# Kernel optimization log

Hardware: AMD Instinct MI355X
Metric: run time of the kernel (lower is better)

## Reference

```python
import jax, jax.numpy as jnp
import numpy as np

D_MODEL = 256
GAMMA = 0.9          # ret_D is built in the torch forward but never applied to the output; kept for fidelity notes
SCALE_BASE = 512     # XPOS default
TEMP = 10000.0
TWO_PI = 2.0 * np.pi


def sine_pos_embed(x):
    """DETR-style 1D sine position embedding with an all-ones mask (as in forward).
    x: [B,T,C] -> pos: [1,T,C] (mask is [1,T] ones, so batch dim broadcasts)."""
    T, C = x.shape[1], x.shape[2]
    x_embed = jnp.arange(1, T + 1, dtype=jnp.float32)          # cumsum of ones
    x_embed = x_embed / (x_embed[-1] + 1e-6) * TWO_PI          # normalize=True
    dim_t = TEMP ** (2.0 * (jnp.arange(C) // 2).astype(jnp.float32) / C)
    pos = x_embed[:, None] / dim_t                             # [T,C]
    pos = jnp.stack([jnp.sin(pos[:, 0::2]), jnp.cos(pos[:, 1::2])], axis=2).reshape(T, C)
    return pos[None].astype(x.dtype)


def _dup_interleave(m):
    # [L, d/2] -> [L, d], columns repeated pairwise: [a,b] -> [a,a,b,b]
    return jnp.repeat(m, 2, axis=-1)


def _rotate_every_two(x):
    x1, x2 = x[..., 0::2], x[..., 1::2]
    return jnp.stack([-x2, x1], axis=-1).reshape(x.shape)


def xpos_apply(x, downscale=False):
    """RetNet XPOS rotary embedding. x: [B,L,d]."""
    L, d = x.shape[1], x.shape[2]
    half = d // 2
    scale_vec = (jnp.arange(0, d, 2, dtype=jnp.float32) + 0.4 * d) / (1.4 * d)   # [d/2]
    power = jnp.arange(L, dtype=jnp.float32) / SCALE_BASE
    scale = scale_vec[None, :] ** power[:, None]                                  # [L, d/2]
    inv_freq = 1.0 / (TEMP ** (jnp.arange(half, dtype=jnp.float32) / half))
    sinusoid = jnp.arange(L, dtype=jnp.float32)[:, None] * inv_freq[None, :]      # [L, d/2]
    sin, cos = jnp.sin(sinusoid), jnp.cos(sinusoid)
    if downscale:
        scale = 1.0 / scale
    sin_s = _dup_interleave(sin * scale)[None].astype(x.dtype)   # [1,L,d]
    cos_s = _dup_interleave(cos * scale)[None].astype(x.dtype)
    return x * cos_s + _rotate_every_two(x) * sin_s


def setup_inputs() -> dict:
    key = jax.random.key(0)
    ks = jax.random.split(key, 8)
    B, TXT, VID, D = 16, 32, 2048, D_MODEL
    S = TXT + VID
    inp = {
        "src": jax.random.normal(ks[0], (B, S, D), dtype=jnp.float32),
        "learn_vid_ret": jax.random.normal(ks[1], (VID * VID, 1), dtype=jnp.float32),
        "W_txt_Q": jax.random.normal(ks[2], (D, D), dtype=jnp.float32) / D,
        "W_txt_K": jax.random.normal(ks[3], (D, D), dtype=jnp.float32) / D,
        "W_txt_V": jax.random.normal(ks[4], (D, D), dtype=jnp.float32) / D,
        "W_vid_Q": jax.random.normal(ks[5], (D, D), dtype=jnp.float32) / D,
        "W_vid_K": jax.random.normal(ks[6], (D, D), dtype=jnp.float32) / D,
        "W_vid_V": jax.random.normal(ks[7], (D, D), dtype=jnp.float32) / D,
        "txt_length": TXT,
    }
    return inp


def reference(src, learn_vid_ret, W_txt_Q, W_txt_K, W_txt_V, W_vid_Q, W_vid_K, W_vid_V, txt_length):
    S = src.shape[1]
    vid_length = S - txt_length

    # learned retention mask over the video block
    learn_ret = jax.nn.sigmoid(learn_vid_ret.reshape(vid_length, vid_length))
    diag = jnp.eye(vid_length, dtype=src.dtype)
    video_ret = (1.0 - diag) * learn_ret
    loss_sparsity = jnp.mean(jnp.abs(video_ret))

    # full [S,S] mask: ones everywhere, sigmoid(learned) on the vid-vid block
    ret_mask = jnp.ones((S, S), dtype=src.dtype).at[txt_length:, txt_length:].set(learn_ret)

    txt_mem = src[:, :txt_length]   # [B,TXT,D]
    vid_mem = src[:, txt_length:]   # [B,VID,D]

    pos = sine_pos_embed(txt_mem)   # [1,TXT,D]
    txt_Q = (pos + txt_mem) @ W_txt_Q
    txt_K = (pos + txt_mem) @ W_txt_K
    vid_Q = xpos_apply(vid_mem @ W_vid_Q)
    vid_K = xpos_apply(vid_mem @ W_vid_K, downscale=True)

    Q = jnp.concatenate([txt_Q, vid_Q], axis=1)                  # [B,S,D]
    K = jnp.concatenate([txt_K, vid_K], axis=1)                  # [B,S,D]
    V = jnp.concatenate([txt_mem @ W_txt_V, vid_mem @ W_vid_V], axis=1)

    # retention: QK^T elementwise-masked (no softmax), then weighted V sum
    scores = jnp.einsum('bsd,btd->bst', Q, K) * ret_mask[None]   # [B,S,S]
    out = scores @ V                                             # [B,S,D]
    return out, loss_sparsity
```

## Files before the change

### kernel.cpp

```cpp
#include <hip/hip_runtime.h>

#define B_   16
#define TXT  32
#define VID  2048
#define D_   256
#define S_   2080
#define SP   2176
#define NKT  34
#define GTOT 17424

typedef unsigned short ushort_t;
typedef __attribute__((ext_vector_type(8))) short short8;
typedef __attribute__((ext_vector_type(4))) short short4v;
typedef __attribute__((ext_vector_type(4))) float f32x4;
typedef __attribute__((ext_vector_type(16))) float f32x16;

__device__ __forceinline__ ushort_t f2bf(float f) {
  unsigned u = __builtin_bit_cast(unsigned, f);
  unsigned r = (u + 0x7FFFu + ((u >> 16) & 1u)) >> 16;
  return (ushort_t)r;
}
__device__ __forceinline__ float bf2f(ushort_t h) {
  unsigned u = ((unsigned)h) << 16;
  return __builtin_bit_cast(float, u);
}

__device__ __forceinline__ void g2l16(void* lds, const void* g) {
  __builtin_amdgcn_global_load_lds(
      (const __attribute__((address_space(1))) char*)g,
      (__attribute__((address_space(3))) char*)lds, 16, 0, 0);
}

__device__ __forceinline__ f32x4 mfma16(short8 a, short8 b, f32x4 c) {
  return __builtin_amdgcn_mfma_f32_16x16x32_bf16(a, b, c, 0, 0, 0);
}
__device__ __forceinline__ f32x16 mfma32(short8 a, short8 b, f32x16 c) {
  return __builtin_amdgcn_mfma_f32_32x32x16_bf16(a, b, c, 0, 0, 0);
}


__global__ void prep_kernel(const float* __restrict__ src, const float* __restrict__ learn,
                            const float* __restrict__ Wtq, const float* __restrict__ Wtk,
                            const float* __restrict__ Wtv,
                            const float* __restrict__ Wvq, const float* __restrict__ Wvk,
                            const float* __restrict__ Wvv,
                            ushort_t* __restrict__ Qs, ushort_t* __restrict__ Ks,
                            ushort_t* __restrict__ VTs, ushort_t* __restrict__ sigp,
                            float* __restrict__ tbl, ushort_t* __restrict__ WT,
                            float* __restrict__ loss) {
  __shared__ float shf[64 * 68];
  const int blk = blockIdx.x;
  const int tid = threadIdx.x;

  if (blk < 64) {
    float (*a_s)[256] = (float(*)[256])shf;
    float (*x_s)[256] = (float(*)[256])(shf + 2048);
    const int tg = blk & 3;
    const int b  = blk >> 2;
    const int c  = tid;
    #pragma unroll
    for (int t = 0; t < 8; ++t) {
      int row = tg * 8 + t;
      float x = src[((size_t)b * S_ + row) * D_ + c];
      float xe = (float)(row + 1) * (6.283185307179586f / (32.0f + 1e-6f));
      int i = c >> 1;
      float dimt = powf(10000.0f, (2.0f * (float)i) / 256.0f);
      float ang = xe / dimt;
      float pv = (c & 1) ? cosf(ang) : sinf(ang);
      x_s[t][c] = x;
      a_s[t][c] = x + pv;
    }
    __syncthreads();
    float q[8] = {0,0,0,0,0,0,0,0}, k[8] = {0,0,0,0,0,0,0,0}, v[8] = {0,0,0,0,0,0,0,0};
    for (int kk = 0; kk < 256; ++kk) {
      float wq = Wtq[(size_t)kk * 256 + c];
      float wk = Wtk[(size_t)kk * 256 + c];
      float wv = Wtv[(size_t)kk * 256 + c];
      #pragma unroll
      for (int t = 0; t < 8; ++t) {
        q[t] = fmaf(a_s[t][kk], wq, q[t]);
        k[t] = fmaf(a_s[t][kk], wk, k[t]);
        v[t] = fmaf(x_s[t][kk], wv, v[t]);
      }
    }
    #pragma unroll
    for (int t = 0; t < 8; ++t) {
      int row = tg * 8 + t;
      size_t base = ((size_t)(b * NKT)) << 14;
      size_t sub = (size_t)(c >> 4) * 1024 + row * 16 + (c & 15);
      Qs[base + sub] = f2bf(q[t]);
      Ks[(base + sub) ^ (size_t)(((row >> 2) & 7) << 3)] = f2bf(k[t]);
      VTs[base + (size_t)(row >> 4) * 4096 + c * 16 + (row & 15)] = f2bf(v[t]);
    }
  } else if (blk < 112) {
    float (*t)[68] = (float(*)[68])shf;
    const int m = blk - 64;
    const int k0 = (m & 3) * 64, n0 = ((m >> 2) & 3) * 64, mt = m >> 4;
    const float* W = (mt == 0) ? Wvq : (mt == 1) ? Wvk : Wvv;
    int r = tid >> 4, cq = (tid & 15) * 4;
    #pragma unroll
    for (int mm = 0; mm < 4; ++mm) {
      int k = mm * 16 + r;
      float4 v = *(const float4*)(W + (size_t)(k0 + k) * 256 + n0 + cq);
      t[k][cq] = v.x; t[k][cq + 1] = v.y; t[k][cq + 2] = v.z; t[k][cq + 3] = v.w;
    }
    __syncthreads();
    #pragma unroll
    for (int mm = 0; mm < 4; ++mm) {
      int n = mm * 16 + r;
      short4v h;
      h[0] = (short)f2bf(t[cq + 0][n]);
      h[1] = (short)f2bf(t[cq + 1][n]);
      h[2] = (short)f2bf(t[cq + 2][n]);
      h[3] = (short)f2bf(t[cq + 3][n]);
      *(short4v*)(WT + ((size_t)mt * D_ + n0 + n) * D_ + k0 + cq) = h;
    }
  } else if (blk < 1136) {
    int idx = (blk - 112) * 256 + tid;
    int n = idx >> 7, i = idx & 127;
    float invf = powf(10000.0f, -(float)i / 128.0f);
    float ang = (float)n * invf;
    float s, co;
    sincosf(ang, &s, &co);
    float sv = ((float)(2 * i) + 102.4f) / 358.4f;
    float sc = powf(sv, (float)n / 512.0f);
    float4 r;
    r.x = co * sc; r.y = s * sc; r.z = co / sc; r.w = s / sc;
    *(float4*)(tbl + (size_t)idx * 4) = r;
  } else if (blk < 1328) {
    int i = (blk - 1136) * 256 + tid;
    short8 z = {0, 0, 0, 0, 0, 0, 0, 0};
    int sec = i >> 14;
    int j = i & 16383;
    int bb = j >> 10;
    int rem = j & 1023;
    size_t base = ((size_t)(bb * NKT + 32)) << 14;
    if (sec == 0) {
      int kstep = rem >> 6, ch = rem & 63;
      *(short8*)(Qs + base + kstep * 1024 + 512 + ch * 8) = z;
    } else if (sec == 1) {
      int kstep = rem >> 6, ch = rem & 63;
      *(short8*)(Ks + base + kstep * 1024 + 512 + ch * 8) = z;
    } else {
      *(short8*)(VTs + base + 8192 + rem * 8) = z;
    }
  } else {
    float* red = shf;
    const int base = ((blk - 1328) * 256 + tid) * 8;
    float4 v0 = *(const float4*)(learn + base);
    float4 v1 = *(const float4*)(learn + base + 4);
    float vals[8] = {v0.x, v0.y, v0.z, v0.w, v1.x, v1.y, v1.z, v1.w};
    float acc = 0.f;
    short8 sh;
    #pragma unroll
    for (int j = 0; j < 8; ++j) {
      int idx = base + j;
      float s = 1.0f / (1.0f + expf(-vals[j]));
      sh[j] = (short)f2bf(s);
      int rr = idx >> 11, cc = idx & 2047;
      if (rr != cc) acc += s;
    }
    *(short8*)(sigp + base) = sh;
    red[tid] = acc;
    __syncthreads();
    #pragma unroll
    for (int st = 128; st > 0; st >>= 1) {
      if (tid < st) red[tid] += red[tid + st];
      __syncthreads();
    }
    if (tid == 0) atomicAdd(loss, red[0] * (1.0f / 4194304.0f));
  }
}

__global__ void cvt_kernel(const float* __restrict__ src, ushort_t* __restrict__ srcb) {
  int i = blockIdx.x * 256 + threadIdx.x;
  int b = i >> 16;
  int rem = i & 65535;
  int row = rem >> 5, c8 = (rem & 31) * 8;
  const float* p = src + ((size_t)b * S_ + TXT + row) * D_ + c8;
  float4 v0 = *(const float4*)p;
  float4 v1 = *(const float4*)(p + 4);
  short8 h;
  h[0] = (short)f2bf(v0.x); h[1] = (short)f2bf(v0.y); h[2] = (short)f2bf(v0.z); h[3] = (short)f2bf(v0.w);
  h[4] = (short)f2bf(v1.x); h[5] = (short)f2bf(v1.y); h[6] = (short)f2bf(v1.z); h[7] = (short)f2bf(v1.w);
  *(short8*)(srcb + ((size_t)b * VID + row) * D_ + c8) = h;
}

template <int MODE>
__global__ __launch_bounds__(256, 2) void vid_gemm(
    const float* __restrict__ src, const ushort_t* __restrict__ srcb,
    const ushort_t* __restrict__ WT, const float* __restrict__ tbl,
    ushort_t* __restrict__ Qs, ushort_t* __restrict__ Ks, ushort_t* __restrict__ VTs) {
  __shared__ __align__(16) ushort_t ldsA[64 * 64];
  __shared__ __align__(16) ushort_t ldsB[64 * 64];

  const int rt = blockIdx.x;
  const int b  = blockIdx.y;
  const int ct = blockIdx.z;
  const int nt = ct >> 2;
  const int n0 = (ct & 3) * 64;
  const int tid = threadIdx.x;
  const int wv = tid >> 6, lane = tid & 63, l15 = lane & 15, l4 = lane >> 4;

  f32x4 acc[4];
  #pragma unroll
  for (int t2 = 0; t2 < 4; ++t2) { acc[t2][0] = 0.f; acc[t2][1] = 0.f; acc[t2][2] = 0.f; acc[t2][3] = 0.f; }

  for (int kk = 0; kk < 256; kk += 64) {
    if (MODE == 1) {
      #pragma unroll
      for (int m = 0; m < 2; ++m) {
        int p = (m * 256 + tid) * 16;
        int r = p >> 7;
        int cb = (p & 127) ^ ((r & 7) << 4);
        g2l16((char*)ldsA + p,
              (const char*)(srcb + ((size_t)b * VID + rt * 64 + r) * D_ + kk) + cb);
      }
    } else {
      #pragma unroll
      for (int m = 0; m < 4; ++m) {
        int q = m * 256 + tid;
        int r = q >> 4;
        int kc = (q & 15) * 4;
        const float4 v = *(const float4*)(src + ((size_t)b * S_ + TXT + rt * 64 + r) * D_ + kk + kc);
        short4v h;
        h[0] = (short)f2bf(v.x); h[1] = (short)f2bf(v.y);
        h[2] = (short)f2bf(v.z); h[3] = (short)f2bf(v.w);
        int off = ((r << 7) + (kc << 1)) ^ ((r & 7) << 4);
        *(short4v*)((char*)ldsA + off) = h;
      }
    }
    #pragma unroll
    for (int m = 0; m < 2; ++m) {
      int p = (m * 256 + tid) * 16;
      int nl = p >> 7;
      int c = (p & 127) ^ ((nl & 7) << 4);
      g2l16((char*)ldsB + p, (const char*)(WT + ((size_t)nt * D_ + n0 + nl) * D_ + kk) + c);
    }
    __syncthreads();
    #pragma unroll
    for (int ks = 0; ks < 2; ++ks) {
      int ar = wv * 16 + l15;
      int aoff = ((ar << 7) + ((ks * 32 + l4 * 8) << 1)) ^ ((ar & 7) << 4);
      short8 av = *(const short8*)((const char*)ldsA + aoff);
      #pragma unroll
      for (int t2 = 0; t2 < 4; ++t2) {
        int nl = t2 * 16 + l15;
        int boff = ((nl << 7) + ((ks * 32 + l4 * 8) << 1)) ^ ((nl & 7) << 4);
        short8 bv = *(const short8*)((const char*)ldsB + boff);
        acc[t2] = mfma16(av, bv, acc[t2]);
      }
    }
    __syncthreads();
  }

  const int rowl = wv * 16 + l4 * 4;
  if (nt < 2) {
    #pragma unroll
    for (int t2 = 0; t2 < 4; ++t2) {
      int c = n0 + t2 * 16 + l15;
      #pragma unroll
      for (int r = 0; r < 4; ++r) {
        int n = rt * 64 + rowl + r;
        float x = acc[t2][r];
        float xp = __shfl_xor(x, 1);
        const float4 tb = *(const float4*)(tbl + ((size_t)n * 128 + (c >> 1)) * 4);
        float cs = (nt == 0) ? tb.x : tb.z;
        float ss = (nt == 0) ? tb.y : tb.w;
        float val = (c & 1) ? fmaf(x, cs, xp * ss) : fmaf(x, cs, -xp * ss);
        int rowg = TXT + n;
        size_t idx = (((size_t)(b * NKT + (rowg >> 6))) << 14)
                   + (size_t)(c >> 4) * 1024 + (rowg & 63) * 16 + (c & 15);
        if (nt == 0) Qs[idx] = f2bf(val);
        else         Ks[idx ^ (size_t)(((rowg >> 2) & 7) << 3)] = f2bf(val);
      }
    }
  } else {
    #pragma unroll
    for (int t2 = 0; t2 < 4; ++t2)
      #pragma unroll
      for (int r = 0; r < 4; ++r) {
        int rr = rowl + r;
        int cc = t2 * 16 + l15;
        int off = ((rr << 7) + (cc << 1)) ^ ((rr & 7) << 4);
        *(ushort_t*)((char*)ldsA + off) = f2bf(acc[t2][r]);
      }
    __syncthreads();
    int n = tid >> 2;
    int rc = (tid & 3) * 16;
    short8 o0, o1;
    #pragma unroll
    for (int j = 0; j < 8; ++j) {
      int rr = rc + j;
      int off = ((rr << 7) + (n << 1)) ^ ((rr & 7) << 4);
      o0[j] = *(const short*)((const char*)ldsA + off);
    }
    #pragma unroll
    for (int j = 0; j < 8; ++j) {
      int rr = rc + 8 + j;
      int off = ((rr << 7) + (n << 1)) ^ ((rr & 7) << 4);
      o1[j] = *(const short*)((const char*)ldsA + off);
    }
    int d = n0 + n;
    int kvg0 = TXT + rt * 64 + rc;
    size_t base = (((size_t)(b * NKT + (kvg0 >> 6))) << 14) + ((kvg0 >> 4) & 3) * 4096 + d * 16;
    *(short8*)(VTs + base) = o0;
    *(short8*)(VTs + base + 8) = o1;
  }
}

__global__ __launch_bounds__(256) void attn_kernel(
    const ushort_t* __restrict__ Qs, const ushort_t* __restrict__ Ks,
    const ushort_t* __restrict__ VTs, const ushort_t* __restrict__ sigp,
    float* __restrict__ out) {
  __shared__ __align__(16) ushort_t Kb[16384];
  __shared__ __align__(16) ushort_t Pb[4096];

  const int kblk = blockIdx.x;
  const int bs = (kblk & 7) * 96 + (kblk >> 3);
  int g = bs * 22 + (bs < 528 ? bs : 528);
  const int gend = g + 22 + (bs < 528 ? 1 : 0);

  const int tid = threadIdx.x;
  const int wid = tid >> 6, lane = tid & 63;
  const int l31 = lane & 31, l5 = lane >> 5;
  const int qh = wid >> 1, kh = wid & 1;
  const int d0 = wid * 64;
  const int qloc = qh * 32 + l31;
  const int pswz = (l31 & 7) << 4;
  const int krbase = kh * 32 + l31;
  const int kxor = ((krbase >> 2) & 7) << 4;
  const int krow = krbase * 32 + l5 * 16;

  int b = g / 1089, rem = g - b * 1089, qt = rem / 33, kvt = rem - qt * 33;

  short8 qf[16];
  int4 mq[4];

  auto ldq = [&](int bb, int qq) {
    const ushort_t* qb = Qs + (((size_t)(bb * NKT + qq)) << 14) + qloc * 16 + l5 * 8;
    #pragma unroll
    for (int ks = 0; ks < 16; ++ks) qf[ks] = *(const short8*)(qb + ks * 1024);
  };
  auto ldmask = [&](int qq, int tt) {
    int q = qq * 64 + qloc;
    int qc = q - TXT; qc = qc < 0 ? 0 : (qc > 2047 ? 2047 : qc);
    int kvp = tt * 64 + kh * 32 - TXT;
    int kvc = (kvp >= 0 && kvp <= 2016) ? kvp : 0;
    const int4* mrow = (const int4*)(sigp + (size_t)qc * 2048 + kvc);
    mq[0] = mrow[0]; mq[1] = mrow[1]; mq[2] = mrow[2]; mq[3] = mrow[3];
  };
  auto stageK = [&](int bb, int tt) {
    const char* src = (const char*)Ks + (((size_t)(bb * NKT + tt)) << 15);
    #pragma unroll
    for (int m = 0; m < 8; ++m) { int s2 = m * 256 + tid; g2l16((char*)Kb + s2 * 16, src + s2 * 16); }
  };

  f32x16 oacc[2][2];
  #pragma unroll
  for (int i2 = 0; i2 < 2; ++i2)
    #pragma unroll
    for (int j2 = 0; j2 < 2; ++j2)
      #pragma unroll
      for (int r = 0; r < 16; ++r) oacc[i2][j2][r] = 0.f;

  stageK(b, kvt);
  ldmask(qt, kvt);
  ldq(b, qt);
  asm volatile("s_waitcnt vmcnt(0)" ::: "memory");
  __builtin_amdgcn_sched_barrier(0);
  __builtin_amdgcn_s_barrier();
  __builtin_amdgcn_sched_barrier(0);

  while (g < gend) {
    int n1_b = b, n1_q = qt, n1_k = kvt + 1;
    if (n1_k == 33) { n1_k = 0; ++n1_q; if (n1_q == 33) { n1_q = 0; ++n1_b; } }
    const bool last = (g + 1 == gend);

    f32x16 s0, s1;
    #pragma unroll
    for (int r = 0; r < 16; ++r) { s0[r] = 0.f; s1[r] = 0.f; }
    __builtin_amdgcn_s_setprio(1);
    #pragma unroll
    for (int ks = 0; ks < 8; ++ks) {
      short8 ka = *(const short8*)((const char*)Kb + ((ks * 2048 + krow) ^ kxor));
      short8 kc = *(const short8*)((const char*)Kb + (((ks + 8) * 2048 + krow) ^ kxor));
      s0 = mfma32(ka, qf[ks], s0);
      s1 = mfma32(kc, qf[ks + 8], s1);
    }
    __builtin_amdgcn_s_setprio(0);

    {
      int q = qt * 64 + qloc;
      bool qv = (q >= TXT) && (q < S_);
      int kvp = kvt * 64 + kh * 32 - TXT;
      bool kvv = (kvp >= 0 && kvp <= 2016);
      bool ok = qv && kvv;
      const unsigned* mw = (const unsigned*)mq;
      #pragma unroll
      for (int t = 0; t < 4; ++t) {
        unsigned w0p, w1p;
        {
          unsigned wa = mw[4 * t + 0], wb = mw[4 * t + 2];
          unsigned w = l5 ? wb : wa;
          float m0 = ok ? bf2f((ushort_t)(w & 0xFFFFu)) : 1.0f;
          float m1 = ok ? bf2f((ushort_t)(w >> 16)) : 1.0f;
          int r = 4 * t;
          float p0 = (s0[r] + s1[r]) * m0;
          float p1 = (s0[r + 1] + s1[r + 1]) * m1;
          asm("v_cvt_pk_bf16_f32 %0, %1, %2" : "=v"(w0p) : "v"(p0), "v"(p1));
        }
        {
          unsigned wa = mw[4 * t + 1], wb = mw[4 * t + 3];
          unsigned w = l5 ? wb : wa;
          float m0 = ok ? bf2f((ushort_t)(w & 0xFFFFu)) : 1.0f;
          float m1 = ok ? bf2f((ushort_t)(w >> 16)) : 1.0f;
          int r = 4 * t + 2;
          float p0 = (s0[r] + s1[r]) * m0;
          float p1 = (s0[r + 1] + s1[r + 1]) * m1;
          asm("v_cvt_pk_bf16_f32 %0, %1, %2" : "=v"(w1p) : "v"(p0), "v"(p1));
        }
        int off = ((qloc << 7) + (kh << 6) + (t << 4) + (l5 << 3)) ^ pswz;
        *(uint2*)((char*)Pb + off) = make_uint2(w0p, w1p);
      }
    }

    asm volatile("s_waitcnt lgkmcnt(0)" ::: "memory");
    __builtin_amdgcn_sched_barrier(0);
    __builtin_amdgcn_s_barrier();
    __builtin_amdgcn_sched_barrier(0);

    if (!last) stageK(n1_b, n1_k);

    const ushort_t* vb = VTs + (((size_t)(b * NKT + kvt)) << 14) + (size_t)d0 * 16 + l5 * 8;
    __builtin_amdgcn_s_setprio(1);
    #pragma unroll
    for (int ks = 0; ks < 4; ++ks) {
      short8 vf0 = *(const short8*)(vb + ks * 4096 + l31 * 16);
      short8 vf1 = *(const short8*)(vb + ks * 4096 + (l31 + 32) * 16);
      short8 pf0 = *(const short8*)((const char*)Pb + ((l31 * 128 + ks * 32 + l5 * 16) ^ pswz));
      short8 pf1 = *(const short8*)((const char*)Pb + (((32 + l31) * 128 + ks * 32 + l5 * 16) ^ pswz));
      oacc[0][0] = mfma32(pf0, vf0, oacc[0][0]);
      oacc[0][1] = mfma32(pf0, vf1, oacc[0][1]);
      oacc[1][0] = mfma32(pf1, vf0, oacc[1][0]);
      oacc[1][1] = mfma32(pf1, vf1, oacc[1][1]);
    }
    __builtin_amdgcn_s_setprio(0);
    asm volatile("s_waitcnt lgkmcnt(0)" ::: "memory");
    __builtin_amdgcn_sched_barrier(0);

    if (kvt == 32 || last) {
      #pragma unroll
      for (int qg2 = 0; qg2 < 2; ++qg2)
        #pragma unroll
        for (int dg = 0; dg < 2; ++dg)
          #pragma unroll
          for (int r = 0; r < 16; ++r) {
            int qg = qt * 64 + qg2 * 32 + (r & 3) + 8 * (r >> 2) + 4 * l5;
            int dd = d0 + dg * 32 + l31;
            if (qg < S_)
              unsafeAtomicAdd(&out[((size_t)b * S_ + qg) * D_ + dd], oacc[qg2][dg][r]);
            oacc[qg2][dg][r] = 0.f;
          }
    }

    if (!last) {
      ldmask(n1_q, n1_k);
      if (n1_q != qt || n1_b != b) {
        ldq(n1_b, n1_q);
        asm volatile("s_waitcnt vmcnt(20)" ::: "memory");
      } else {
        asm volatile("s_waitcnt vmcnt(4)" ::: "memory");
      }
    }
    __builtin_amdgcn_sched_barrier(0);
    __builtin_amdgcn_s_barrier();
    __builtin_amdgcn_sched_barrier(0);

    b = n1_b; qt = n1_q; kvt = n1_k; ++g;
  }
}

extern "C" void kernel_launch(void* const* d_in, const int* in_sizes, int n_in,
                              void* d_out, int out_size, void* d_ws, size_t ws_size,
                              hipStream_t stream) {
  (void)in_sizes; (void)n_in;
  const float* src   = (const float*)d_in[0];
  const float* learn = (const float*)d_in[1];
  const float* Wtq = (const float*)d_in[2];
  const float* Wtk = (const float*)d_in[3];
  const float* Wtv = (const float*)d_in[4];
  const float* Wvq = (const float*)d_in[5];
  const float* Wvk = (const float*)d_in[6];
  const float* Wvv = (const float*)d_in[7];
  float* out = (float*)d_out;

  char* ws = (char*)d_ws;
  const size_t QKV_ONE  = (size_t)B_ * SP * D_ * 2;
  const size_t QP_OFF   = 0;
  const size_t KS_OFF   = QP_OFF + QKV_ONE;
  const size_t VT_OFF   = KS_OFF + QKV_ONE;
  const size_t SIG_OFF  = VT_OFF + QKV_ONE;
  const size_t TBL_OFF  = SIG_OFF + (size_t)VID * VID * 2;
  const size_t WT_OFF   = TBL_OFF + (size_t)VID * 128 * 4 * sizeof(float);
  const size_t SRCB_OFF = WT_OFF + (size_t)3 * D_ * D_ * 2;
  const size_t NEED_SRCB = SRCB_OFF + (size_t)B_ * VID * D_ * 2;

  ushort_t* Qs   = (ushort_t*)(ws + QP_OFF);
  ushort_t* Ks   = (ushort_t*)(ws + KS_OFF);
  ushort_t* VTs  = (ushort_t*)(ws + VT_OFF);
  ushort_t* sigp = (ushort_t*)(ws + SIG_OFF);
  float*    tbl  = (float*)(ws + TBL_OFF);
  ushort_t* WT   = (ushort_t*)(ws + WT_OFF);
  ushort_t* srcb = (ushort_t*)(ws + SRCB_OFF);
  float*    loss = out + (size_t)B_ * S_ * D_;

  hipMemsetAsync(d_out, 0, (size_t)out_size * sizeof(float), stream);
  prep_kernel<<<3376, 256, 0, stream>>>(src, learn, Wtq, Wtk, Wtv, Wvq, Wvk, Wvv,
                                        Qs, Ks, VTs, sigp, tbl, WT, loss);
  if (ws_size >= NEED_SRCB) {
    cvt_kernel<<<4096, 256, 0, stream>>>(src, srcb);
    vid_gemm<1><<<dim3(32, B_, 12), 256, 0, stream>>>(src, srcb, WT, tbl, Qs, Ks, VTs);
  } else {
    vid_gemm<0><<<dim3(32, B_, 12), 256, 0, stream>>>(src, srcb, WT, tbl, Qs, Ks, VTs);
  }
  attn_kernel<<<dim3(768), 256, 0, stream>>>(Qs, Ks, VTs, sigp, out);
}
```

Before: 354.0 us.

## Fuse bf16 conversion into projection GEMM and stage V through LDS in attention

The projection GEMM now loads a full 64x256 row tile of the video source into LDS once, converting to bf16 there, and loops over all 12 output column tiles. This removes the separate conversion kernel and repeated A-tile reloads. The attention kernel stages V tiles into LDS asynchronously alongside K, drops the K XOR swizzle, and switches to 512 blocks with two blocks per CU and a different work partition. The risks are more LDS per block, lower occupancy, and far fewer blocks for the projection GEMM (512 instead of 6144).

```diff
diff --git a/kernel.cpp b/kernel.cpp
--- a/kernel.cpp
+++ b/kernel.cpp
@@ -89,7 +89,7 @@
       size_t base = ((size_t)(b * NKT)) << 14;
       size_t sub = (size_t)(c >> 4) * 1024 + row * 16 + (c & 15);
       Qs[base + sub] = f2bf(q[t]);
-      Ks[(base + sub) ^ (size_t)(((row >> 2) & 7) << 3)] = f2bf(k[t]);
+      Ks[base + sub] = f2bf(k[t]);
       VTs[base + (size_t)(row >> 4) * 4096 + c * 16 + (row & 15)] = f2bf(v[t]);
     }
   } else if (blk < 112) {
@@ -172,154 +172,135 @@
   }
 }
 
-__global__ void cvt_kernel(const float* __restrict__ src, ushort_t* __restrict__ srcb) {
-  int i = blockIdx.x * 256 + threadIdx.x;
-  int b = i >> 16;
-  int rem = i & 65535;
-  int row = rem >> 5, c8 = (rem & 31) * 8;
-  const float* p = src + ((size_t)b * S_ + TXT + row) * D_ + c8;
-  float4 v0 = *(const float4*)p;
-  float4 v1 = *(const float4*)(p + 4);
-  short8 h;
-  h[0] = (short)f2bf(v0.x); h[1] = (short)f2bf(v0.y); h[2] = (short)f2bf(v0.z); h[3] = (short)f2bf(v0.w);
-  h[4] = (short)f2bf(v1.x); h[5] = (short)f2bf(v1.y); h[6] = (short)f2bf(v1.z); h[7] = (short)f2bf(v1.w);
-  *(short8*)(srcb + ((size_t)b * VID + row) * D_ + c8) = h;
-}
-
-template <int MODE>
 __global__ __launch_bounds__(256, 2) void vid_gemm(
-    const float* __restrict__ src, const ushort_t* __restrict__ srcb,
-    const ushort_t* __restrict__ WT, const float* __restrict__ tbl,
+    const float* __restrict__ src, const ushort_t* __restrict__ WT,
+    const float* __restrict__ tbl,
     ushort_t* __restrict__ Qs, ushort_t* __restrict__ Ks, ushort_t* __restrict__ VTs) {
-  __shared__ __align__(16) ushort_t ldsA[64 * 64];
+  __shared__ __align__(16) ushort_t ldsA[64 * 256];
   __shared__ __align__(16) ushort_t ldsB[64 * 64];
 
   const int rt = blockIdx.x;
   const int b  = blockIdx.y;
-  const int ct = blockIdx.z;
-  const int nt = ct >> 2;
-  const int n0 = (ct & 3) * 64;
   const int tid = threadIdx.x;
   const int wv = tid >> 6, lane = tid & 63, l15 = lane & 15, l4 = lane >> 4;
 
-  f32x4 acc[4];
   #pragma unroll
-  for (int t2 = 0; t2 < 4; ++t2) { acc[t2][0] = 0.f; acc[t2][1] = 0.f; acc[t2][2] = 0.f; acc[t2][3] = 0.f; }
-
-  for (int kk = 0; kk < 256; kk += 64) {
-    if (MODE == 1) {
+  for (int m = 0; m < 16; ++m) {
+    int idx = m * 256 + tid;
+    int r = idx >> 6;
+    int c4 = (idx & 63) * 4;
+    const float4 v = *(const float4*)(src + ((size_t)b * S_ + TXT + rt * 64 + r) * D_ + c4);
+    short4v h;
+    h[0] = (short)f2bf(v.x); h[1] = (short)f2bf(v.y);
+    h[2] = (short)f2bf(v.z); h[3] = (short)f2bf(v.w);
+    int off = ((r << 9) + (c4 << 1)) ^ ((r & 7) << 4);
+    *(short4v*)((char*)ldsA + off) = h;
+  }
+  __syncthreads();
+
+  for (int ct = 0; ct < 12; ++ct) {
+    const int nt = ct >> 2;
+    const int n0 = (ct & 3) * 64;
+
+    f32x4 acc[4];
+    #pragma unroll
+    for (int t2 = 0; t2 < 4; ++t2) { acc[t2][0] = 0.f; acc[t2][1] = 0.f; acc[t2][2] = 0.f; acc[t2][3] = 0.f; }
+
+    for (int k4 = 0; k4 < 4; ++k4) {
+      const int kk = k4 * 64;
       #pragma unroll
       for (int m = 0; m < 2; ++m) {
         int p = (m * 256 + tid) * 16;
-        int r = p >> 7;
-        int cb = (p & 127) ^ ((r & 7) << 4);
-        g2l16((char*)ldsA + p,
-              (const char*)(srcb + ((size_t)b * VID + rt * 64 + r) * D_ + kk) + cb);
+        int nl = p >> 7;
+        int c = (p & 127) ^ ((nl & 7) << 4);
+        g2l16((char*)ldsB + p, (const char*)(WT + ((size_t)nt * D_ + n0 + nl) * D_ + kk) + c);
+      }
+      __syncthreads();
+      #pragma unroll
+      for (int ks = 0; ks < 2; ++ks) {
+        int ar = wv * 16 + l15;
+        int aoff = ((ar << 9) + ((kk + ks * 32 + l4 * 8) << 1)) ^ ((ar & 7) << 4);
+        short8 av = *(const short8*)((const char*)ldsA + aoff);
+        #pragma unroll
+        for (int t2 = 0; t2 < 4; ++t2) {
+          int nl = t2 * 16 + l15;
+          int boff = ((nl << 7) + ((ks * 32 + l4 * 8) << 1)) ^ ((nl & 7) << 4);
+          short8 bv = *(const short8*)((const char*)ldsB + boff);
+          acc[t2] = mfma16(av, bv, acc[t2]);
+        }
+      }
+      __syncthreads();
+    }
+
+    const int rowl = wv * 16 + l4 * 4;
+    if (nt < 2) {
+      #pragma unroll
+      for (int t2 = 0; t2 < 4; ++t2) {
+        int c = n0 + t2 * 16 + l15;
+        #pragma unroll
+        for (int r = 0; r < 4; ++r) {
+          int n = rt * 64 + rowl + r;
+          float x = acc[t2][r];
+          float xp = __shfl_xor(x, 1);
+          const float4 tb = *(const float4*)(tbl + ((size_t)n * 128 + (c >> 1)) * 4);
+          float cs = (nt == 0) ? tb.x : tb.z;
+          float ss = (nt == 0) ? tb.y : tb.w;
+          float val = (c & 1) ? fmaf(x, cs, xp * ss) : fmaf(x, cs, -xp * ss);
+          int rowg = TXT + n;
+          size_t idx = (((size_t)(b * NKT + (rowg >> 6))) << 14)
+                     + (size_t)(c >> 4) * 1024 + (rowg & 63) * 16 + (c & 15);
+          if (nt == 0) Qs[idx] = f2bf(val);
+          else         Ks[idx] = f2bf(val);
+        }
       }
     } else {
       #pragma unroll
-      for (int m = 0; m < 4; ++m) {
-        int q = m * 256 + tid;
-        int r = q >> 4;
-        int kc = (q & 15) * 4;
-        const float4 v = *(const float4*)(src + ((size_t)b * S_ + TXT + rt * 64 + r) * D_ + kk + kc);
-        short4v h;
-        h[0] = (short)f2bf(v.x); h[1] = (short)f2bf(v.y);
-        h[2] = (short)f2bf(v.z); h[3] = (short)f2bf(v.w);
-        int off = ((r << 7) + (kc << 1)) ^ ((r & 7) << 4);
-        *(short4v*)((char*)ldsA + off) = h;
-      }
-    }
-    #pragma unroll
-    for (int m = 0; m < 2; ++m) {
-      int p = (m * 256 + tid) * 16;
-      int nl = p >> 7;
-      int c = (p & 127) ^ ((nl & 7) << 4);
-      g2l16((char*)ldsB + p, (const char*)(WT + ((size_t)nt * D_ + n0 + nl) * D_ + kk) + c);
-    }
-    __syncthreads();
-    #pragma unroll
-    for (int ks = 0; ks < 2; ++ks) {
-      int ar = wv * 16 + l15;
-      int aoff = ((ar << 7) + ((ks * 32 + l4 * 8) << 1)) ^ ((ar & 7) << 4);
-      short8 av = *(const short8*)((const char*)ldsA + aoff);
-      #pragma unroll
-      for (int t2 = 0; t2 < 4; ++t2) {
-        int nl = t2 * 16 + l15;
-        int boff = ((nl << 7) + ((ks * 32 + l4 * 8) << 1)) ^ ((nl & 7) << 4);
-        short8 bv = *(const short8*)((const char*)ldsB + boff);
-        acc[t2] = mfma16(av, bv, acc[t2]);
-      }
-    }
-    __syncthreads();
+      for (int t2 = 0; t2 < 4; ++t2)
+        #pragma unroll
+        for (int r = 0; r < 4; ++r) {
+          int rr = rowl + r;
+          int cc = t2 * 16 + l15;
+          int off = ((rr << 7) + (cc << 1)) ^ ((rr & 7) << 4);
+          *(ushort_t*)((char*)ldsB + off) = f2bf(acc[t2][r]);
+        }
+      __syncthreads();
+      int n = tid >> 2;
+      int rc = (tid & 3) * 16;
+      short8 o0, o1;
+      #pragma unroll
+      for (int j = 0; j < 8; ++j) {
+        int rr = rc + j;
+        int off = ((rr << 7) + (n << 1)) ^ ((rr & 7) << 4);
+        o0[j] = *(const short*)((const char*)ldsB + off);
+      }
+      #pragma unroll
+      for (int j = 0; j < 8; ++j) {
+        int rr = rc + 8 + j;
+        int off = ((rr << 7) + (n << 1)) ^ ((rr & 7) << 4);
+        o1[j] = *(const short*)((const char*)ldsB + off);
+      }
+      int d = n0 + n;
+      int kvg0 = TXT + rt * 64 + rc;
+      size_t base = (((size_t)(b * NKT + (kvg0 >> 6))) << 14) + ((kvg0 >> 4) & 3) * 4096 + d * 16;
+      *(short8*)(VTs + base) = o0;
+      *(short8*)(VTs + base + 8) = o1;
+      __syncthreads();
+    }
   }
-
-  const int rowl = wv * 16 + l4 * 4;
-  if (nt < 2) {
-    #pragma unroll
-    for (int t2 = 0; t2 < 4; ++t2) {
-      int c = n0 + t2 * 16 + l15;
-      #pragma unroll
-      for (int r = 0; r < 4; ++r) {
-        int n = rt * 64 + rowl + r;
-        float x = acc[t2][r];
-        float xp = __shfl_xor(x, 1);
-        const float4 tb = *(const float4*)(tbl + ((size_t)n * 128 + (c >> 1)) * 4);
-        float cs = (nt == 0) ? tb.x : tb.z;
-        float ss = (nt == 0) ? tb.y : tb.w;
-        float val = (c & 1) ? fmaf(x, cs, xp * ss) : fmaf(x, cs, -xp * ss);
-        int rowg = TXT + n;
-        size_t idx = (((size_t)(b * NKT + (rowg >> 6))) << 14)
-                   + (size_t)(c >> 4) * 1024 + (rowg & 63) * 16 + (c & 15);
-        if (nt == 0) Qs[idx] = f2bf(val);
-        else         Ks[idx ^ (size_t)(((rowg >> 2) & 7) << 3)] = f2bf(val);
-      }
-    }
-  } else {
-    #pragma unroll
-    for (int t2 = 0; t2 < 4; ++t2)
-      #pragma unroll
-      for (int r = 0; r < 4; ++r) {
-        int rr = rowl + r;
-        int cc = t2 * 16 + l15;
-        int off = ((rr << 7) + (cc << 1)) ^ ((rr & 7) << 4);
-        *(ushort_t*)((char*)ldsA + off) = f2bf(acc[t2][r]);
-      }
-    __syncthreads();
-    int n = tid >> 2;
-    int rc = (tid & 3) * 16;
-    short8 o0, o1;
-    #pragma unroll
-    for (int j = 0; j < 8; ++j) {
-      int rr = rc + j;
-      int off = ((rr << 7) + (n << 1)) ^ ((rr & 7) << 4);
-      o0[j] = *(const short*)((const char*)ldsA + off);
-    }
-    #pragma unroll
-    for (int j = 0; j < 8; ++j) {
-      int rr = rc + 8 + j;
-      int off = ((rr << 7) + (n << 1)) ^ ((rr & 7) << 4);
-      o1[j] = *(const short*)((const char*)ldsA + off);
-    }
-    int d = n0 + n;
-    int kvg0 = TXT + rt * 64 + rc;
-    size_t base = (((size_t)(b * NKT + (kvg0 >> 6))) << 14) + ((kvg0 >> 4) & 3) * 4096 + d * 16;
-    *(short8*)(VTs + base) = o0;
-    *(short8*)(VTs + base + 8) = o1;
-  }
-}
-
-__global__ __launch_bounds__(256) void attn_kernel(
+}
+
+__global__ __launch_bounds__(256, 2) void attn_kernel(
     const ushort_t* __restrict__ Qs, const ushort_t* __restrict__ Ks,
     const ushort_t* __restrict__ VTs, const ushort_t* __restrict__ sigp,
     float* __restrict__ out) {
   __shared__ __align__(16) ushort_t Kb[16384];
+  __shared__ __align__(16) ushort_t Vb[16384];
   __shared__ __align__(16) ushort_t Pb[4096];
 
   const int kblk = blockIdx.x;
-  const int bs = (kblk & 7) * 96 + (kblk >> 3);
-  int g = bs * 22 + (bs < 528 ? bs : 528);
-  const int gend = g + 22 + (bs < 528 ? 1 : 0);
+  const int bs = (kblk & 7) * 64 + (kblk >> 3);
+  int g = bs * 34 + (bs >> 5);
+  const int gend = (bs + 1) * 34 + ((bs + 1) >> 5);
 
   const int tid = threadIdx.x;
   const int wid = tid >> 6, lane = tid & 63;
@@ -328,9 +309,6 @@
   const int d0 = wid * 64;
   const int qloc = qh * 32 + l31;
   const int pswz = (l31 & 7) << 4;
-  const int krbase = kh * 32 + l31;
-  const int kxor = ((krbase >> 2) & 7) << 4;
-  const int krow = krbase * 32 + l5 * 16;
 
   int b = g / 1089, rem = g - b * 1089, qt = rem / 33, kvt = rem - qt * 33;
 
@@ -355,6 +333,11 @@
     #pragma unroll
     for (int m = 0; m < 8; ++m) { int s2 = m * 256 + tid; g2l16((char*)Kb + s2 * 16, src + s2 * 16); }
   };
+  auto stageV = [&](int bb, int tt) {
+    const char* src = (const char*)VTs + (((size_t)(bb * NKT + tt)) << 15);
+    #pragma unroll
+    for (int m = 0; m < 8; ++m) { int s2 = m * 256 + tid; g2l16((char*)Vb + s2 * 16, src + s2 * 16); }
+  };
 
   f32x16 oacc[2][2];
   #pragma unroll
@@ -364,8 +347,24 @@
       #pragma unroll
       for (int r = 0; r < 16; ++r) oacc[i2][j2][r] = 0.f;
 
+  auto flushO = [&](int bb, int qq) {
+    #pragma unroll
+    for (int qg2 = 0; qg2 < 2; ++qg2)
+      #pragma unroll
+      for (int dg = 0; dg < 2; ++dg)
+        #pragma unroll
+        for (int r = 0; r < 16; ++r) {
+          int qg = qq * 64 + qg2 * 32 + (r & 3) + 8 * (r >> 2) + 4 * l5;
+          int dd = d0 + dg * 32 + l31;
+          if (qg < S_)
+            unsafeAtomicAdd(&out[((size_t)bb * S_ + qg) * D_ + dd], oacc[qg2][dg][r]);
+          oacc[qg2][dg][r] = 0.f;
+        }
+  };
+
   stageK(b, kvt);
   ldmask(qt, kvt);
+  stageV(b, kvt);
   ldq(b, qt);
   asm volatile("s_waitcnt vmcnt(0)" ::: "memory");
   __builtin_amdgcn_sched_barrier(0);
@@ -373,18 +372,18 @@
   __builtin_amdgcn_sched_barrier(0);
 
   while (g < gend) {
-    int n1_b = b, n1_q = qt, n1_k = kvt + 1;
-    if (n1_k == 33) { n1_k = 0; ++n1_q; if (n1_q == 33) { n1_q = 0; ++n1_b; } }
-    const bool last = (g + 1 == gend);
+    int gn = (g + 1 < GTOT) ? g + 1 : GTOT - 1;
+    int nb = gn / 1089, nrem = gn - nb * 1089, nqt = nrem / 33, nkvt = nrem - nqt * 33;
 
     f32x16 s0, s1;
     #pragma unroll
     for (int r = 0; r < 16; ++r) { s0[r] = 0.f; s1[r] = 0.f; }
+    const int arow = (kh * 32 + l31) * 32 + l5 * 16;
     __builtin_amdgcn_s_setprio(1);
     #pragma unroll
     for (int ks = 0; ks < 8; ++ks) {
-      short8 ka = *(const short8*)((const char*)Kb + ((ks * 2048 + krow) ^ kxor));
-      short8 kc = *(const short8*)((const char*)Kb + (((ks + 8) * 2048 + krow) ^ kxor));
+      short8 ka = *(const short8*)((const char*)Kb + ks * 2048 + arow);
+      short8 kc = *(const short8*)((const char*)Kb + (ks + 8) * 2048 + arow);
       s0 = mfma32(ka, qf[ks], s0);
       s1 = mfma32(kc, qf[ks + 8], s1);
     }
@@ -425,21 +424,23 @@
       }
     }
 
-    asm volatile("s_waitcnt lgkmcnt(0)" ::: "memory");
+    asm volatile("s_waitcnt vmcnt(0) lgkmcnt(0)" ::: "memory");
     __builtin_amdgcn_sched_barrier(0);
     __builtin_amdgcn_s_barrier();
     __builtin_amdgcn_sched_barrier(0);
 
-    if (!last) stageK(n1_b, n1_k);
-
-    const ushort_t* vb = VTs + (((size_t)(b * NKT + kvt)) << 14) + (size_t)d0 * 16 + l5 * 8;
+    stageK(nb, nkvt);
+    __builtin_amdgcn_sched_barrier(0);
+
     __builtin_amdgcn_s_setprio(1);
     #pragma unroll
     for (int ks = 0; ks < 4; ++ks) {
-      short8 vf0 = *(const short8*)(vb + ks * 4096 + l31 * 16);
-      short8 vf1 = *(const short8*)(vb + ks * 4096 + (l31 + 32) * 16);
-      short8 pf0 = *(const short8*)((const char*)Pb + ((l31 * 128 + ks * 32 + l5 * 16) ^ pswz));
-      short8 pf1 = *(const short8*)((const char*)Pb + (((32 + l31) * 128 + ks * 32 + l5 * 16) ^ pswz));
+      int p0 = (l31 * 128 + ks * 32 + l5 * 16) ^ pswz;
+      int p1 = ((32 + l31) * 128 + ks * 32 + l5 * 16) ^ pswz;
+      short8 pf0 = *(const short8*)((const char*)Pb + p0);
+      short8 pf1 = *(const short8*)((const char*)Pb + p1);
+      short8 vf0 = *(const short8*)((const char*)Vb + ks * 8192 + (d0 + l31) * 32 + l5 * 16);
+      short8 vf1 = *(const short8*)((const char*)Vb + ks * 8192 + (d0 + 32 + l31) * 32 + l5 * 16);
       oacc[0][0] = mfma32(pf0, vf0, oacc[0][0]);
       oacc[0][1] = mfma32(pf0, vf1, oacc[0][1]);
       oacc[1][0] = mfma32(pf1, vf0, oacc[1][0]);
@@ -448,43 +449,35 @@
     __builtin_amdgcn_s_setprio(0);
     asm volatile("s_waitcnt lgkmcnt(0)" ::: "memory");
     __builtin_amdgcn_sched_barrier(0);
-
-    if (kvt == 32 || last) {
-      #pragma unroll
-      for (int qg2 = 0; qg2 < 2; ++qg2)
-        #pragma unroll
-        for (int dg = 0; dg < 2; ++dg)
-          #pragma unroll
-          for (int r = 0; r < 16; ++r) {
-            int qg = qt * 64 + qg2 * 32 + (r & 3) + 8 * (r >> 2) + 4 * l5;
-            int dd = d0 + dg * 32 + l31;
-            if (qg < S_)
-              unsafeAtomicAdd(&out[((size_t)b * S_ + qg) * D_ + dd], oacc[qg2][dg][r]);
-            oacc[qg2][dg][r] = 0.f;
-          }
-    }
-
-    if (!last) {
-      ldmask(n1_q, n1_k);
-      if (n1_q != qt || n1_b != b) {
-        ldq(n1_b, n1_q);
-        asm volatile("s_waitcnt vmcnt(20)" ::: "memory");
-      } else {
-        asm volatile("s_waitcnt vmcnt(4)" ::: "memory");
-      }
-    }
-    __builtin_amdgcn_sched_barrier(0);
     __builtin_amdgcn_s_barrier();
     __builtin_amdgcn_sched_barrier(0);
 
-    b = n1_b; qt = n1_q; kvt = n1_k; ++g;
+    ldmask(nqt, nkvt);
+    __builtin_amdgcn_sched_barrier(0);
+    const bool qchange = (nqt != qt || nb != b);
+    if (qchange) {
+      flushO(b, qt);
+      ldq(nb, nqt);
+    }
+    __builtin_amdgcn_sched_barrier(0);
+    stageV(nb, nkvt);
+    __builtin_amdgcn_sched_barrier(0);
+    if (qchange) { asm volatile("s_waitcnt vmcnt(24)" ::: "memory"); }
+    else         { asm volatile("s_waitcnt vmcnt(12)" ::: "memory"); }
+    __builtin_amdgcn_sched_barrier(0);
+    __builtin_amdgcn_s_barrier();
+    __builtin_amdgcn_sched_barrier(0);
+
+    b = nb; qt = nqt; kvt = nkvt; ++g;
   }
+
+  flushO(b, qt);
 }
 
 extern "C" void kernel_launch(void* const* d_in, const int* in_sizes, int n_in,
                               void* d_out, int out_size, void* d_ws, size_t ws_size,
                               hipStream_t stream) {
-  (void)in_sizes; (void)n_in;
+  (void)in_sizes; (void)n_in; (void)ws_size;
   const float* src   = (const float*)d_in[0];
   const float* learn = (const float*)d_in[1];
   const float* Wtq = (const float*)d_in[2];
@@ -503,8 +496,6 @@
   const size_t SIG_OFF  = VT_OFF + QKV_ONE;
   const size_t TBL_OFF  = SIG_OFF + (size_t)VID * VID * 2;
   const size_t WT_OFF   = TBL_OFF + (size_t)VID * 128 * 4 * sizeof(float);
-  const size_t SRCB_OFF = WT_OFF + (size_t)3 * D_ * D_ * 2;
-  const size_t NEED_SRCB = SRCB_OFF + (size_t)B_ * VID * D_ * 2;
 
   ushort_t* Qs   = (ushort_t*)(ws + QP_OFF);
   ushort_t* Ks   = (ushort_t*)(ws + KS_OFF);
@@ -512,17 +503,11 @@
   ushort_t* sigp = (ushort_t*)(ws + SIG_OFF);
   float*    tbl  = (float*)(ws + TBL_OFF);
   ushort_t* WT   = (ushort_t*)(ws + WT_OFF);
-  ushort_t* srcb = (ushort_t*)(ws + SRCB_OFF);
   float*    loss = out + (size_t)B_ * S_ * D_;
 
   hipMemsetAsync(d_out, 0, (size_t)out_size * sizeof(float), stream);
   prep_kernel<<<3376, 256, 0, stream>>>(src, learn, Wtq, Wtk, Wtv, Wvq, Wvk, Wvv,
                                         Qs, Ks, VTs, sigp, tbl, WT, loss);
-  if (ws_size >= NEED_SRCB) {
-    cvt_kernel<<<4096, 256, 0, stream>>>(src, srcb);
-    vid_gemm<1><<<dim3(32, B_, 12), 256, 0, stream>>>(src, srcb, WT, tbl, Qs, Ks, VTs);
-  } else {
-    vid_gemm<0><<<dim3(32, B_, 12), 256, 0, stream>>>(src, srcb, WT, tbl, Qs, Ks, VTs);
-  }
-  attn_kernel<<<dim3(768), 256, 0, stream>>>(Qs, Ks, VTs, sigp, out);
-}
+  vid_gemm<<<dim3(32, B_), 256, 0, stream>>>(src, WT, tbl, Qs, Ks, VTs);
+  attn_kernel<<<dim3(512), 256, 0, stream>>>(Qs, Ks, VTs, sigp, out);
+}
```

New measurement: 316.6 us. -10.5%, faster.
